# Performance work log

Measured on AMD Instinct MI355X. Metric: run time of the kernel, lower is better.

## Reference

```python
import jax, jax.numpy as jnp
import numpy as np

B, T, E, H, QKV = 4, 2048, 1024, 16, 64
D = E // H  # head_dim = 64


def setup_inputs() -> dict:
    key = jax.random.key(0)
    k1, k2, k3, k4 = jax.random.split(key, 4)
    scale = 1.0 / np.sqrt(D)
    x = jax.random.normal(k1, (B, T, E), dtype=jnp.float32)
    W_q = jax.random.normal(k2, (QKV, D), dtype=jnp.float32) * scale
    W_k = jax.random.normal(k3, (QKV, D), dtype=jnp.float32) * scale
    W_v = jax.random.normal(k4, (QKV, D), dtype=jnp.float32) * scale
    return {"x": x, "W_q": W_q, "W_k": W_k, "W_v": W_v}


def reference(x, W_q, W_k, W_v):
    Bx, Tx, Ex = x.shape
    d = Ex // H
    # [B,T,E] -> [B,H,T,D]  (same as torch view + permute(0,2,1,3))
    xh = x.reshape(Bx, Tx, H, d).transpose(0, 2, 1, 3)
    # Shared per-head projections: Linear(d -> qkv_dim), weight stored [out,in]
    Q = jnp.einsum("bhtd,qd->bhtq", xh, W_q)
    K = jnp.einsum("bhtd,qd->bhtq", xh, W_k)
    V = jnp.einsum("bhtd,qd->bhtq", xh, W_v)
    # NOTE: original scales by head_dim**0.5, not qkv_dim**0.5
    scores = jnp.einsum("bhtq,bhsq->bhts", Q, K) / jnp.asarray(d, x.dtype) ** 0.5
    attn = jax.nn.softmax(scores, axis=-1)
    out = jnp.einsum("bhts,bhsq->bhtq", attn, V) + V  # attention + V residual
    # per-head concat on last dim == head-major merge: [B,H,T,Q] -> [B,T,H*Q]
    return out.transpose(0, 2, 1, 3).reshape(Bx, Tx, H * W_q.shape[0])
```

## Files before the change

### kernel.cpp

```cpp
#include <hip/hip_runtime.h>

#define T_SEQ 2048
#define N_B   4
#define N_H   16
#define D_H   64
#define EMB   1024
#define CSC   0.18033688011f

typedef __attribute__((ext_vector_type(8))) short   vshort8;
typedef __attribute__((ext_vector_type(4))) float   vfloat4;
typedef __attribute__((ext_vector_type(16))) float  vfloat16;

__device__ __forceinline__ ushort f2bf(float f) {
  union { float f; unsigned u; } v; v.f = f;
  unsigned u = v.u;
  return (ushort)((u + 0x7fffu + ((u >> 16) & 1u)) >> 16);
}
__device__ __forceinline__ unsigned pk2bf(float a, float b) {
  return (unsigned)f2bf(a) | ((unsigned)f2bf(b) << 16);
}
__device__ __forceinline__ float bf2f(ushort b) {
  union { unsigned u; float f; } v; v.u = ((unsigned)b) << 16;
  return v.f;
}
__device__ __forceinline__ float fexp2(float x) {
#if __has_builtin(__builtin_amdgcn_exp2f)
  return __builtin_amdgcn_exp2f(x);
#else
  return exp2f(x);
#endif
}
__device__ __forceinline__ unsigned permhi(float hi, float lo) {
  union { float f; unsigned u; } a, b; a.f = hi; b.f = lo;
#if __has_builtin(__builtin_amdgcn_perm)
  return __builtin_amdgcn_perm(a.u, b.u, 0x07060302u);
#else
  return (a.u & 0xFFFF0000u) | (b.u >> 16);
#endif
}
__device__ __forceinline__ vshort8 cvt8(const float* p) {
  float4 w0 = *(const float4*)(p);
  float4 w1 = *(const float4*)(p + 4);
  vshort8 t;
  t[0] = (short)f2bf(w0.x); t[1] = (short)f2bf(w0.y);
  t[2] = (short)f2bf(w0.z); t[3] = (short)f2bf(w0.w);
  t[4] = (short)f2bf(w1.x); t[5] = (short)f2bf(w1.y);
  t[6] = (short)f2bf(w1.z); t[7] = (short)f2bf(w1.w);
  return t;
}


__global__ void wconv(const float* __restrict__ Wq, const float* __restrict__ Wk,
                      const float* __restrict__ Wv, ushort* __restrict__ Wb) {
  const int lane = threadIdx.x & 63;
  const int l15  = lane & 15;
  const int quad = lane >> 4;
  const float* Ws[3] = {Wq, Wk, Wv};
#pragma unroll
  for (int m = 0; m < 3; ++m)
#pragma unroll
    for (int kc = 0; kc < 2; ++kc)
#pragma unroll
      for (int nt = 0; nt < 4; ++nt) {
        vshort8 t = cvt8(Ws[m] + (nt * 16 + l15) * D_H + kc * 32 + quad * 8);
        *(vshort8*)(&Wb[(((m * 2 + kc) * 4 + nt) * 64 + lane) * 8]) = t;
      }
}

__global__ __launch_bounds__(256, 4) void proj_qkv(
    const float* __restrict__ x, const ushort* __restrict__ Wb,
    uint2* __restrict__ Qb, uint2* __restrict__ Kb, uint2* __restrict__ Vb) {
  const int wid  = threadIdx.x >> 6;
  const int lane = threadIdx.x & 63;
  const int l15  = lane & 15;
  const int q    = lane >> 4;
  const int gw    = blockIdx.x * 4 + wid;
  const int strip = gw >> 4;
  const int hd    = gw & 15;
  const int r0    = strip * 16;
  const int b     = r0 >> 11;
  const int bh    = b * N_H + hd;
  const int ts    = (r0 & (T_SEQ - 1)) >> 4;

  vshort8 afr[2];
  {
    const float* xp = x + (size_t)(r0 + l15) * EMB + hd * D_H + q * 8;
    afr[0] = cvt8(xp);
    afr[1] = cvt8(xp + 32);
  }

  uint2* Bs[3] = {Qb, Kb, Vb};
#pragma unroll
  for (int m = 0; m < 3; ++m) {
    vshort8 wf[2][4];
#pragma unroll
    for (int kc = 0; kc < 2; ++kc)
#pragma unroll
      for (int nt = 0; nt < 4; ++nt)
        wf[kc][nt] = *(const vshort8*)(&Wb[(((m * 2 + kc) * 4 + nt) * 64 + lane) * 8]);
    vfloat4 acc[4];
#pragma unroll
    for (int nt = 0; nt < 4; ++nt) acc[nt] = (vfloat4){0.f, 0.f, 0.f, 0.f};
#pragma unroll
    for (int kc = 0; kc < 2; ++kc)
#pragma unroll
      for (int nt = 0; nt < 4; ++nt)
        acc[nt] = (m < 2)
          ? __builtin_amdgcn_mfma_f32_16x16x32_bf16(wf[kc][nt], afr[kc], acc[nt], 0, 0, 0)
          : __builtin_amdgcn_mfma_f32_16x16x32_bf16(afr[kc], wf[kc][nt], acc[nt], 0, 0, 0);
    uint2* B = Bs[m];
#pragma unroll
    for (int nt = 0; nt < 4; ++nt) {
      vfloat4 a = acc[nt];
      if (m == 0) { a[0] *= CSC; a[1] *= CSC; a[2] *= CSC; a[3] *= CSC; }
      uint2 w;
      w.x = pk2bf(a[0], a[1]);
      w.y = pk2bf(a[2], a[3]);
      size_t idx;
      if (m < 2) {
        idx = ((size_t)(bh * 64 + (ts >> 1)) * 4 + nt) * 128
              + (l15 + 16 * (ts & 1)) * 4 + q;
      } else {
        idx = (((size_t)(bh * 32 + (ts >> 2)) * 4 + (ts & 3)) * 2 + (nt >> 1)) * 128
              + 64 * (nt & 1) + l15 * 4 + q;
      }
      B[idx] = w;
    }
  }
}

__global__ __launch_bounds__(256, 2) void attn_fused(
    const uint4* __restrict__ Qb, const uint4* __restrict__ Kb,
    const uint4* __restrict__ Vb, float* __restrict__ out) {
  const int tid  = threadIdx.x;
  const int wid  = tid >> 6;
  const int lane = tid & 63;
  const int l31  = lane & 31;
  const int h    = lane >> 5;

  const int blk  = blockIdx.x;
  const int work = (blk & 7) * 64 + (blk >> 3);
  const int bh   = work >> 3;
  const int tblk8 = work & 7;
  const int b = bh >> 4, hh = bh & 15;
  const int T64 = tblk8 * 4 + wid;

  const int lo = l31 * 2 + h;

  vshort8 qf[2][4];
#pragma unroll
  for (int tb = 0; tb < 2; ++tb)
#pragma unroll
    for (int ds = 0; ds < 4; ++ds)
      qf[tb][ds] = *(const vshort8*)&Qb[((size_t)(bh * 64 + 2 * T64 + tb) * 4 + ds) * 64 + lo];

  vfloat16 oacc[2][2];
#pragma unroll
  for (int tb = 0; tb < 2; ++tb)
#pragma unroll
    for (int db = 0; db < 2; ++db)
#pragma unroll
      for (int i = 0; i < 16; ++i) oacc[tb][db][i] = 0.f;
  float lsum[2] = {0.f, 0.f};

#pragma unroll 1
  for (int ss = 0; ss < 32; ++ss) {
    vshort8 kf[2][4];
#pragma unroll
    for (int sb = 0; sb < 2; ++sb)
#pragma unroll
      for (int ds = 0; ds < 4; ++ds)
        kf[sb][ds] = *(const vshort8*)&Kb[((size_t)(bh * 64 + 2 * ss + sb) * 4 + ds) * 64 + lo];
    vshort8 vf[4][2];
#pragma unroll
    for (int st = 0; st < 4; ++st)
#pragma unroll
      for (int db = 0; db < 2; ++db)
        vf[st][db] = *(const vshort8*)&Vb[(((size_t)(bh * 32 + ss) * 4 + st) * 2 + db) * 64 + lo];

#pragma unroll
    for (int tb = 0; tb < 2; ++tb) {
      vfloat16 sacc[2];
#pragma unroll
      for (int sb = 0; sb < 2; ++sb) {
#pragma unroll
        for (int i = 0; i < 16; ++i) sacc[sb][i] = 0.f;
#pragma unroll
        for (int ds = 0; ds < 4; ++ds)
          sacc[sb] = __builtin_amdgcn_mfma_f32_32x32x16_bf16(kf[sb][ds], qf[tb][ds], sacc[sb], 0, 0, 0);
      }
      float p[2][16];
      float ls = 0.f;
#pragma unroll
      for (int sb = 0; sb < 2; ++sb)
#pragma unroll
        for (int r = 0; r < 16; ++r) {
          p[sb][r] = fexp2(sacc[sb][r]);
          ls += p[sb][r];
        }
      lsum[tb] += ls;

#pragma unroll
      for (int sb = 0; sb < 2; ++sb)
#pragma unroll
        for (int g = 0; g < 2; ++g) {
          const unsigned OL0 = permhi(p[sb][8 * g + 1], p[sb][8 * g + 0]);
          const unsigned OL1 = permhi(p[sb][8 * g + 3], p[sb][8 * g + 2]);
          const unsigned OH0 = permhi(p[sb][8 * g + 5], p[sb][8 * g + 4]);
          const unsigned OH1 = permhi(p[sb][8 * g + 7], p[sb][8 * g + 6]);
          const unsigned s0 = h ? OL0 : OH0;
          const unsigned s1 = h ? OL1 : OH1;
          const unsigned r0 = (unsigned)__shfl_xor((int)s0, 32, 64);
          const unsigned r1 = (unsigned)__shfl_xor((int)s1, 32, 64);
          union { unsigned u[4]; vshort8 v; } pa;
          pa.u[0] = h ? r0 : OL0;
          pa.u[1] = h ? r1 : OL1;
          pa.u[2] = h ? OH0 : r0;
          pa.u[3] = h ? OH1 : r1;
          const int st = 2 * sb + g;
#pragma unroll
          for (int db = 0; db < 2; ++db)
            oacc[tb][db] = __builtin_amdgcn_mfma_f32_32x32x16_bf16(pa.v, vf[st][db], oacc[tb][db], 0, 0, 0);
        }
    }
  }

  const uint2* Vb2 = (const uint2*)Vb;
#pragma unroll
  for (int tb = 0; tb < 2; ++tb) {
    const float l = lsum[tb] + __shfl_xor(lsum[tb], 32, 64);
    const float inv = 1.0f / l;
    const int T32 = 2 * T64 + tb;
#pragma unroll
    for (int db = 0; db < 2; ++db) {
#pragma unroll
      for (int rq = 0; rq < 4; ++rq) {
        const int sq = 8 * T32 + 2 * rq + h;
        uint2 vr = Vb2[(((size_t)(bh * 32 + (sq >> 4)) * 4 + ((sq >> 2) & 3)) * 2 + db) * 128
                       + l31 * 4 + ((sq >> 1) & 1) * 2 + (sq & 1)];
        float vres[4];
        vres[0] = bf2f((ushort)(vr.x & 0xFFFFu));
        vres[1] = bf2f((ushort)(vr.x >> 16));
        vres[2] = bf2f((ushort)(vr.y & 0xFFFFu));
        vres[3] = bf2f((ushort)(vr.y >> 16));
#pragma unroll
        for (int rr = 0; rr < 4; ++rr) {
          const int row = rr + 8 * rq + 4 * h;
          const float iT = __shfl(inv, row, 64);
          const int t = T32 * 32 + row;
          out[((size_t)(b * T_SEQ + t)) * EMB + hh * D_H + db * 32 + l31] =
              oacc[tb][db][rq * 4 + rr] * iT + vres[rr];
        }
      }
    }
  }
}

extern "C" void kernel_launch(void* const* d_in, const int* in_sizes, int n_in,
                              void* d_out, int out_size, void* d_ws, size_t ws_size,
                              hipStream_t stream) {
  const float* x  = (const float*)d_in[0];
  const float* Wq = (const float*)d_in[1];
  const float* Wk = (const float*)d_in[2];
  const float* Wv = (const float*)d_in[3];
  float* out = (float*)d_out;

  const size_t per4 = (size_t)64 * 64 * 4 * 64;
  uint4* Qb = (uint4*)d_ws;
  uint4* Kb = Qb + per4;
  uint4* Vb = Kb + per4;
  ushort* Wb = (ushort*)(Vb + per4);

  wconv<<<1, 64, 0, stream>>>(Wq, Wk, Wv, Wb);
  proj_qkv<<<2048, 256, 0, stream>>>(x, Wb, (uint2*)Qb, (uint2*)Kb, (uint2*)Vb);
  attn_fused<<<512, 256, 0, stream>>>(Qb, Kb, Vb, out);
}
```

Baseline: 175.8 us.

## Halve per-wave query tile, double grid, use permlane32 swap and setprio

Each wave now processes one 32-row query tile instead of two, and the grid doubles to 1024 blocks with launch bounds raised to 3 blocks per CU. The goals are lower register pressure, higher occupancy and finer load balance. The cross-half shuffle of probabilities is replaced by v_permlane32_swap, and s_setprio wraps the MFMA groups to favour matrix issue. The cost is that each K/V tile loaded per wave is now reused for half as many query rows, which doubles K/V global traffic.

```diff
diff --git a/kernel.cpp b/kernel.cpp
--- a/kernel.cpp
+++ b/kernel.cpp
@@ -37,6 +37,9 @@
 #else
   return (a.u & 0xFFFF0000u) | (b.u >> 16);
 #endif
+}
+__device__ __forceinline__ void plswap(unsigned &a, unsigned &b) {
+  asm("v_permlane32_swap_b32 %0, %1" : "+v"(a), "+v"(b));
 }
 __device__ __forceinline__ vshort8 cvt8(const float* p) {
   float4 w0 = *(const float4*)(p);
@@ -129,7 +132,7 @@
   }
 }
 
-__global__ __launch_bounds__(256, 2) void attn_fused(
+__global__ __launch_bounds__(256, 3) void attn_fused(
     const uint4* __restrict__ Qb, const uint4* __restrict__ Kb,
     const uint4* __restrict__ Vb, float* __restrict__ out) {
   const int tid  = threadIdx.x;
@@ -139,29 +142,25 @@
   const int h    = lane >> 5;
 
   const int blk  = blockIdx.x;
-  const int work = (blk & 7) * 64 + (blk >> 3);
-  const int bh   = work >> 3;
-  const int tblk8 = work & 7;
+  const int work = (blk & 7) * 128 + (blk >> 3);
+  const int bh   = work >> 4;
+  const int tblk = work & 15;
   const int b = bh >> 4, hh = bh & 15;
-  const int T64 = tblk8 * 4 + wid;
+  const int T32 = tblk * 4 + wid;
 
   const int lo = l31 * 2 + h;
 
-  vshort8 qf[2][4];
-#pragma unroll
-  for (int tb = 0; tb < 2; ++tb)
-#pragma unroll
-    for (int ds = 0; ds < 4; ++ds)
-      qf[tb][ds] = *(const vshort8*)&Qb[((size_t)(bh * 64 + 2 * T64 + tb) * 4 + ds) * 64 + lo];
-
-  vfloat16 oacc[2][2];
-#pragma unroll
-  for (int tb = 0; tb < 2; ++tb)
-#pragma unroll
-    for (int db = 0; db < 2; ++db)
-#pragma unroll
-      for (int i = 0; i < 16; ++i) oacc[tb][db][i] = 0.f;
-  float lsum[2] = {0.f, 0.f};
+  vshort8 qf[4];
+#pragma unroll
+  for (int ds = 0; ds < 4; ++ds)
+    qf[ds] = *(const vshort8*)&Qb[((size_t)(bh * 64 + T32) * 4 + ds) * 64 + lo];
+
+  vfloat16 oacc[2];
+#pragma unroll
+  for (int db = 0; db < 2; ++db)
+#pragma unroll
+    for (int i = 0; i < 16; ++i) oacc[db][i] = 0.f;
+  float lsum = 0.f;
 
 #pragma unroll 1
   for (int ss = 0; ss < 32; ++ss) {
@@ -179,78 +178,69 @@
         vf[st][db] = *(const vshort8*)&Vb[(((size_t)(bh * 32 + ss) * 4 + st) * 2 + db) * 64 + lo];
 
 #pragma unroll
-    for (int tb = 0; tb < 2; ++tb) {
-      vfloat16 sacc[2];
-#pragma unroll
-      for (int sb = 0; sb < 2; ++sb) {
-#pragma unroll
-        for (int i = 0; i < 16; ++i) sacc[sb][i] = 0.f;
-#pragma unroll
-        for (int ds = 0; ds < 4; ++ds)
-          sacc[sb] = __builtin_amdgcn_mfma_f32_32x32x16_bf16(kf[sb][ds], qf[tb][ds], sacc[sb], 0, 0, 0);
-      }
-      float p[2][16];
-      float ls = 0.f;
-#pragma unroll
-      for (int sb = 0; sb < 2; ++sb)
-#pragma unroll
-        for (int r = 0; r < 16; ++r) {
-          p[sb][r] = fexp2(sacc[sb][r]);
-          ls += p[sb][r];
-        }
-      lsum[tb] += ls;
-
-#pragma unroll
-      for (int sb = 0; sb < 2; ++sb)
-#pragma unroll
-        for (int g = 0; g < 2; ++g) {
-          const unsigned OL0 = permhi(p[sb][8 * g + 1], p[sb][8 * g + 0]);
-          const unsigned OL1 = permhi(p[sb][8 * g + 3], p[sb][8 * g + 2]);
-          const unsigned OH0 = permhi(p[sb][8 * g + 5], p[sb][8 * g + 4]);
-          const unsigned OH1 = permhi(p[sb][8 * g + 7], p[sb][8 * g + 6]);
-          const unsigned s0 = h ? OL0 : OH0;
-          const unsigned s1 = h ? OL1 : OH1;
-          const unsigned r0 = (unsigned)__shfl_xor((int)s0, 32, 64);
-          const unsigned r1 = (unsigned)__shfl_xor((int)s1, 32, 64);
-          union { unsigned u[4]; vshort8 v; } pa;
-          pa.u[0] = h ? r0 : OL0;
-          pa.u[1] = h ? r1 : OL1;
-          pa.u[2] = h ? OH0 : r0;
-          pa.u[3] = h ? OH1 : r1;
-          const int st = 2 * sb + g;
-#pragma unroll
-          for (int db = 0; db < 2; ++db)
-            oacc[tb][db] = __builtin_amdgcn_mfma_f32_32x32x16_bf16(pa.v, vf[st][db], oacc[tb][db], 0, 0, 0);
-        }
+    for (int sb = 0; sb < 2; ++sb) {
+      vfloat16 sacc;
+#pragma unroll
+      for (int i = 0; i < 16; ++i) sacc[i] = 0.f;
+      __builtin_amdgcn_s_setprio(1);
+#pragma unroll
+      for (int ds = 0; ds < 4; ++ds)
+        sacc = __builtin_amdgcn_mfma_f32_32x32x16_bf16(kf[sb][ds], qf[ds], sacc, 0, 0, 0);
+      __builtin_amdgcn_s_setprio(0);
+
+      float p[16];
+      float s0 = 0.f, s1 = 0.f, s2 = 0.f, s3 = 0.f;
+#pragma unroll
+      for (int r = 0; r < 16; r += 4) {
+        p[r + 0] = fexp2(sacc[r + 0]); s0 += p[r + 0];
+        p[r + 1] = fexp2(sacc[r + 1]); s1 += p[r + 1];
+        p[r + 2] = fexp2(sacc[r + 2]); s2 += p[r + 2];
+        p[r + 3] = fexp2(sacc[r + 3]); s3 += p[r + 3];
+      }
+      lsum += (s0 + s1) + (s2 + s3);
+
+#pragma unroll
+      for (int g = 0; g < 2; ++g) {
+        unsigned OL0 = permhi(p[8 * g + 1], p[8 * g + 0]);
+        unsigned OL1 = permhi(p[8 * g + 3], p[8 * g + 2]);
+        unsigned OH0 = permhi(p[8 * g + 5], p[8 * g + 4]);
+        unsigned OH1 = permhi(p[8 * g + 7], p[8 * g + 6]);
+        plswap(OL0, OH0);
+        plswap(OL1, OH1);
+        union { unsigned u[4]; vshort8 v; } pa;
+        pa.u[0] = OL0; pa.u[1] = OL1; pa.u[2] = OH0; pa.u[3] = OH1;
+        const int st = 2 * sb + g;
+        __builtin_amdgcn_s_setprio(1);
+#pragma unroll
+        for (int db = 0; db < 2; ++db)
+          oacc[db] = __builtin_amdgcn_mfma_f32_32x32x16_bf16(pa.v, vf[st][db], oacc[db], 0, 0, 0);
+        __builtin_amdgcn_s_setprio(0);
+      }
     }
   }
 
   const uint2* Vb2 = (const uint2*)Vb;
-#pragma unroll
-  for (int tb = 0; tb < 2; ++tb) {
-    const float l = lsum[tb] + __shfl_xor(lsum[tb], 32, 64);
-    const float inv = 1.0f / l;
-    const int T32 = 2 * T64 + tb;
-#pragma unroll
-    for (int db = 0; db < 2; ++db) {
-#pragma unroll
-      for (int rq = 0; rq < 4; ++rq) {
-        const int sq = 8 * T32 + 2 * rq + h;
-        uint2 vr = Vb2[(((size_t)(bh * 32 + (sq >> 4)) * 4 + ((sq >> 2) & 3)) * 2 + db) * 128
-                       + l31 * 4 + ((sq >> 1) & 1) * 2 + (sq & 1)];
-        float vres[4];
-        vres[0] = bf2f((ushort)(vr.x & 0xFFFFu));
-        vres[1] = bf2f((ushort)(vr.x >> 16));
-        vres[2] = bf2f((ushort)(vr.y & 0xFFFFu));
-        vres[3] = bf2f((ushort)(vr.y >> 16));
-#pragma unroll
-        for (int rr = 0; rr < 4; ++rr) {
-          const int row = rr + 8 * rq + 4 * h;
-          const float iT = __shfl(inv, row, 64);
-          const int t = T32 * 32 + row;
-          out[((size_t)(b * T_SEQ + t)) * EMB + hh * D_H + db * 32 + l31] =
-              oacc[tb][db][rq * 4 + rr] * iT + vres[rr];
-        }
+  const float l = lsum + __shfl_xor(lsum, 32, 64);
+  const float inv = 1.0f / l;
+#pragma unroll
+  for (int db = 0; db < 2; ++db) {
+#pragma unroll
+    for (int rq = 0; rq < 4; ++rq) {
+      const int sq = 8 * T32 + 2 * rq + h;
+      uint2 vr = Vb2[(((size_t)(bh * 32 + (sq >> 4)) * 4 + ((sq >> 2) & 3)) * 2 + db) * 128
+                     + l31 * 4 + ((sq >> 1) & 1) * 2 + (sq & 1)];
+      float vres[4];
+      vres[0] = bf2f((ushort)(vr.x & 0xFFFFu));
+      vres[1] = bf2f((ushort)(vr.x >> 16));
+      vres[2] = bf2f((ushort)(vr.y & 0xFFFFu));
+      vres[3] = bf2f((ushort)(vr.y >> 16));
+#pragma unroll
+      for (int rr = 0; rr < 4; ++rr) {
+        const int row = rr + 8 * rq + 4 * h;
+        const float iT = __shfl(inv, row, 64);
+        const int t = T32 * 32 + row;
+        out[((size_t)(b * T_SEQ + t)) * EMB + hh * D_H + db * 32 + l31] =
+            oacc[db][rq * 4 + rr] * iT + vres[rr];
       }
     }
   }
@@ -273,5 +263,5 @@
 
   wconv<<<1, 64, 0, stream>>>(Wq, Wk, Wv, Wb);
   proj_qkv<<<2048, 256, 0, stream>>>(x, Wb, (uint2*)Qb, (uint2*)Kb, (uint2*)Vb);
-  attn_fused<<<512, 256, 0, stream>>>(Qb, Kb, Vb, out);
-}
+  attn_fused<<<1024, 256, 0, stream>>>(Qb, Kb, Vb, out);
+}
```

Result: slower. 182.8 us (+4.0%).

## Split key range across wave pairs, reduce partials via LDS, use permlane swap

Applied to the files above, without the earlier changes.

Each block now covers two 64-row query chunks instead of four. Each chunk's key loop is split between two waves, and the halves are combined through shared memory before the epilogue, which doubles the grid to 1024 blocks and raises launch bounds to 3 blocks per SM. The cross-half shuffle and selects are replaced by v_permlane32_swap, s_setprio is placed around the MFMA groups, and the row-sum accumulation is split into four independent chains. The aim is more parallelism and occupancy on the attention kernel, at the cost of an LDS reduction, a barrier and tighter register limits.

```diff
diff --git a/kernel.cpp b/kernel.cpp
--- a/kernel.cpp
+++ b/kernel.cpp
@@ -37,6 +37,9 @@
 #else
   return (a.u & 0xFFFF0000u) | (b.u >> 16);
 #endif
+}
+__device__ __forceinline__ void plswap(unsigned &a, unsigned &b) {
+  asm("v_permlane32_swap_b32 %0, %1" : "+v"(a), "+v"(b));
 }
 __device__ __forceinline__ vshort8 cvt8(const float* p) {
   float4 w0 = *(const float4*)(p);
@@ -129,7 +132,7 @@
   }
 }
 
-__global__ __launch_bounds__(256, 2) void attn_fused(
+__global__ __launch_bounds__(256, 3) void attn_fused(
     const uint4* __restrict__ Qb, const uint4* __restrict__ Kb,
     const uint4* __restrict__ Vb, float* __restrict__ out) {
   const int tid  = threadIdx.x;
@@ -137,13 +140,15 @@
   const int lane = tid & 63;
   const int l31  = lane & 31;
   const int h    = lane >> 5;
+  const int chunk = wid & 1;
+  const int sh    = wid >> 1;
 
   const int blk  = blockIdx.x;
-  const int work = (blk & 7) * 64 + (blk >> 3);
-  const int bh   = work >> 3;
-  const int tblk8 = work & 7;
+  const int work = (blk & 7) * 128 + (blk >> 3);
+  const int bh   = work >> 4;
+  const int tblk = work & 15;
   const int b = bh >> 4, hh = bh & 15;
-  const int T64 = tblk8 * 4 + wid;
+  const int T64 = tblk * 2 + chunk;
 
   const int lo = l31 * 2 + h;
 
@@ -164,7 +169,7 @@
   float lsum[2] = {0.f, 0.f};
 
 #pragma unroll 1
-  for (int ss = 0; ss < 32; ++ss) {
+  for (int ss = sh * 16; ss < sh * 16 + 16; ++ss) {
     vshort8 kf[2][4];
 #pragma unroll
     for (int sb = 0; sb < 2; ++sb)
@@ -182,74 +187,104 @@
     for (int tb = 0; tb < 2; ++tb) {
       vfloat16 sacc[2];
 #pragma unroll
-      for (int sb = 0; sb < 2; ++sb) {
+      for (int sb = 0; sb < 2; ++sb)
 #pragma unroll
         for (int i = 0; i < 16; ++i) sacc[sb][i] = 0.f;
+      __builtin_amdgcn_s_setprio(1);
+#pragma unroll
+      for (int sb = 0; sb < 2; ++sb)
 #pragma unroll
         for (int ds = 0; ds < 4; ++ds)
           sacc[sb] = __builtin_amdgcn_mfma_f32_32x32x16_bf16(kf[sb][ds], qf[tb][ds], sacc[sb], 0, 0, 0);
-      }
+      __builtin_amdgcn_s_setprio(0);
+
       float p[2][16];
-      float ls = 0.f;
+      float s0 = 0.f, s1 = 0.f, s2 = 0.f, s3 = 0.f;
 #pragma unroll
       for (int sb = 0; sb < 2; ++sb)
 #pragma unroll
-        for (int r = 0; r < 16; ++r) {
-          p[sb][r] = fexp2(sacc[sb][r]);
-          ls += p[sb][r];
+        for (int r = 0; r < 16; r += 4) {
+          p[sb][r + 0] = fexp2(sacc[sb][r + 0]); s0 += p[sb][r + 0];
+          p[sb][r + 1] = fexp2(sacc[sb][r + 1]); s1 += p[sb][r + 1];
+          p[sb][r + 2] = fexp2(sacc[sb][r + 2]); s2 += p[sb][r + 2];
+          p[sb][r + 3] = fexp2(sacc[sb][r + 3]); s3 += p[sb][r + 3];
         }
-      lsum[tb] += ls;
+      lsum[tb] += (s0 + s1) + (s2 + s3);
 
 #pragma unroll
       for (int sb = 0; sb < 2; ++sb)
 #pragma unroll
         for (int g = 0; g < 2; ++g) {
-          const unsigned OL0 = permhi(p[sb][8 * g + 1], p[sb][8 * g + 0]);
-          const unsigned OL1 = permhi(p[sb][8 * g + 3], p[sb][8 * g + 2]);
-          const unsigned OH0 = permhi(p[sb][8 * g + 5], p[sb][8 * g + 4]);
-          const unsigned OH1 = permhi(p[sb][8 * g + 7], p[sb][8 * g + 6]);
-          const unsigned s0 = h ? OL0 : OH0;
-          const unsigned s1 = h ? OL1 : OH1;
-          const unsigned r0 = (unsigned)__shfl_xor((int)s0, 32, 64);
-          const unsigned r1 = (unsigned)__shfl_xor((int)s1, 32, 64);
+          unsigned OL0 = permhi(p[sb][8 * g + 1], p[sb][8 * g + 0]);
+          unsigned OL1 = permhi(p[sb][8 * g + 3], p[sb][8 * g + 2]);
+          unsigned OH0 = permhi(p[sb][8 * g + 5], p[sb][8 * g + 4]);
+          unsigned OH1 = permhi(p[sb][8 * g + 7], p[sb][8 * g + 6]);
+          plswap(OL0, OH0);
+          plswap(OL1, OH1);
           union { unsigned u[4]; vshort8 v; } pa;
-          pa.u[0] = h ? r0 : OL0;
-          pa.u[1] = h ? r1 : OL1;
-          pa.u[2] = h ? OH0 : r0;
-          pa.u[3] = h ? OH1 : r1;
+          pa.u[0] = OL0; pa.u[1] = OL1; pa.u[2] = OH0; pa.u[3] = OH1;
           const int st = 2 * sb + g;
+          __builtin_amdgcn_s_setprio(1);
 #pragma unroll
           for (int db = 0; db < 2; ++db)
             oacc[tb][db] = __builtin_amdgcn_mfma_f32_32x32x16_bf16(pa.v, vf[st][db], oacc[tb][db], 0, 0, 0);
+          __builtin_amdgcn_s_setprio(0);
         }
     }
   }
 
-  const uint2* Vb2 = (const uint2*)Vb;
-#pragma unroll
-  for (int tb = 0; tb < 2; ++tb) {
-    const float l = lsum[tb] + __shfl_xor(lsum[tb], 32, 64);
-    const float inv = 1.0f / l;
-    const int T32 = 2 * T64 + tb;
-#pragma unroll
-    for (int db = 0; db < 2; ++db) {
-#pragma unroll
-      for (int rq = 0; rq < 4; ++rq) {
-        const int sq = 8 * T32 + 2 * rq + h;
-        uint2 vr = Vb2[(((size_t)(bh * 32 + (sq >> 4)) * 4 + ((sq >> 2) & 3)) * 2 + db) * 128
-                       + l31 * 4 + ((sq >> 1) & 1) * 2 + (sq & 1)];
-        float vres[4];
-        vres[0] = bf2f((ushort)(vr.x & 0xFFFFu));
-        vres[1] = bf2f((ushort)(vr.x >> 16));
-        vres[2] = bf2f((ushort)(vr.y & 0xFFFFu));
-        vres[3] = bf2f((ushort)(vr.y >> 16));
-#pragma unroll
-        for (int rr = 0; rr < 4; ++rr) {
-          const int row = rr + 8 * rq + 4 * h;
-          const float iT = __shfl(inv, row, 64);
-          const int t = T32 * 32 + row;
-          out[((size_t)(b * T_SEQ + t)) * EMB + hh * D_H + db * 32 + l31] =
-              oacc[tb][db][rq * 4 + rr] * iT + vres[rr];
+  __shared__ float sO[2][64][64];
+  __shared__ float sL[2][2][64];
+  if (sh == 0) {
+#pragma unroll
+    for (int tb = 0; tb < 2; ++tb) {
+      sL[chunk][tb][lane] = lsum[tb];
+#pragma unroll
+      for (int db = 0; db < 2; ++db)
+#pragma unroll
+        for (int i = 0; i < 16; ++i)
+          sO[chunk][(tb * 2 + db) * 16 + i][lane] = oacc[tb][db][i];
+    }
+  }
+  __syncthreads();
+
+  if (sh == 1) {
+#pragma unroll
+    for (int tb = 0; tb < 2; ++tb) {
+      lsum[tb] += sL[chunk][tb][lane];
+#pragma unroll
+      for (int db = 0; db < 2; ++db)
+#pragma unroll
+        for (int i = 0; i < 16; ++i)
+          oacc[tb][db][i] += sO[chunk][(tb * 2 + db) * 16 + i][lane];
+    }
+
+    const uint2* Vb2 = (const uint2*)Vb;
+#pragma unroll
+    for (int tb = 0; tb < 2; ++tb) {
+      const float l = lsum[tb] + __shfl_xor(lsum[tb], 32, 64);
+      const float inv = 1.0f / l;
+      const int T32 = 2 * T64 + tb;
+#pragma unroll
+      for (int db = 0; db < 2; ++db) {
+#pragma unroll
+        for (int rq = 0; rq < 4; ++rq) {
+          const int sq = 8 * T32 + 2 * rq + h;
+          uint2 vr = Vb2[(((size_t)(bh * 32 + (sq >> 4)) * 4 + ((sq >> 2) & 3)) * 2 + db) * 128
+                         + l31 * 4 + ((sq >> 1) & 1) * 2 + (sq & 1)];
+          float vres[4];
+          vres[0] = bf2f((ushort)(vr.x & 0xFFFFu));
+          vres[1] = bf2f((ushort)(vr.x >> 16));
+          vres[2] = bf2f((ushort)(vr.y & 0xFFFFu));
+          vres[3] = bf2f((ushort)(vr.y >> 16));
+#pragma unroll
+          for (int rr = 0; rr < 4; ++rr) {
+            const int row = rr + 8 * rq + 4 * h;
+            const float iT = __shfl(inv, row, 64);
+            const int t = T32 * 32 + row;
+            out[((size_t)(b * T_SEQ + t)) * EMB + hh * D_H + db * 32 + l31] =
+                oacc[tb][db][rq * 4 + rr] * iT + vres[rr];
+          }
         }
       }
     }
@@ -273,5 +308,5 @@
 
   wconv<<<1, 64, 0, stream>>>(Wq, Wk, Wv, Wb);
   proj_qkv<<<2048, 256, 0, stream>>>(x, Wb, (uint2*)Qb, (uint2*)Kb, (uint2*)Vb);
-  attn_fused<<<512, 256, 0, stream>>>(Qb, Kb, Vb, out);
-}
+  attn_fused<<<1024, 256, 0, stream>>>(Qb, Kb, Vb, out);
+}
```

Measured after the change: 645.4 us. 3.67x slower.

## Use permlane32 swap for P repack, add setprio around MFMAs, unroll KV loop

Applied to the files above, without the earlier changes.

Replaces the ds_swizzle/shuffle-based cross-half exchange of the bf16 probability fragments with a v_permlane32_swap instruction, dropping the selects and LDS-path shuffles. It also wraps the MFMA groups in s_setprio to favor matrix issue across waves, and unrolls the KV loop by two with incremented pointers. The first MFMA now takes a zero accumulator instead of explicit zeroing, and the row-sum uses four partial accumulators. It relies on gfx950 permlane32_swap semantics matching the old selection logic and raises register pressure from the unroll.

```diff
diff --git a/kernel.cpp b/kernel.cpp
--- a/kernel.cpp
+++ b/kernel.cpp
@@ -37,6 +37,9 @@
 #else
   return (a.u & 0xFFFF0000u) | (b.u >> 16);
 #endif
+}
+__device__ __forceinline__ void plswap(unsigned &a, unsigned &b) {
+  asm("v_permlane32_swap_b32 %0, %1" : "+v"(a), "+v"(b));
 }
 __device__ __forceinline__ vshort8 cvt8(const float* p) {
   float4 w0 = *(const float4*)(p);
@@ -163,64 +166,77 @@
       for (int i = 0; i < 16; ++i) oacc[tb][db][i] = 0.f;
   float lsum[2] = {0.f, 0.f};
 
-#pragma unroll 1
+  vfloat16 vzero;
+#pragma unroll
+  for (int i = 0; i < 16; ++i) vzero[i] = 0.f;
+
+  const uint4* kp0 = Kb + ((size_t)(bh * 64) * 4) * 64 + lo;
+  const uint4* kp1 = kp0 + 256;
+  const uint4* vp0 = Vb + ((size_t)(bh * 32) * 8) * 64 + lo;
+  const uint4* vp1 = vp0 + 256;
+
+#pragma unroll 2
   for (int ss = 0; ss < 32; ++ss) {
     vshort8 kf[2][4];
 #pragma unroll
-    for (int sb = 0; sb < 2; ++sb)
-#pragma unroll
-      for (int ds = 0; ds < 4; ++ds)
-        kf[sb][ds] = *(const vshort8*)&Kb[((size_t)(bh * 64 + 2 * ss + sb) * 4 + ds) * 64 + lo];
+    for (int ds = 0; ds < 4; ++ds) {
+      kf[0][ds] = *(const vshort8*)&kp0[ds * 64];
+      kf[1][ds] = *(const vshort8*)&kp1[ds * 64];
+    }
     vshort8 vf[4][2];
 #pragma unroll
-    for (int st = 0; st < 4; ++st)
-#pragma unroll
-      for (int db = 0; db < 2; ++db)
-        vf[st][db] = *(const vshort8*)&Vb[(((size_t)(bh * 32 + ss) * 4 + st) * 2 + db) * 64 + lo];
+    for (int st = 0; st < 2; ++st)
+#pragma unroll
+      for (int db = 0; db < 2; ++db) {
+        vf[st][db]     = *(const vshort8*)&vp0[(st * 2 + db) * 64];
+        vf[st + 2][db] = *(const vshort8*)&vp1[(st * 2 + db) * 64];
+      }
+    kp0 += 512; kp1 += 512; vp0 += 512; vp1 += 512;
 
 #pragma unroll
     for (int tb = 0; tb < 2; ++tb) {
       vfloat16 sacc[2];
+      __builtin_amdgcn_s_setprio(1);
 #pragma unroll
       for (int sb = 0; sb < 2; ++sb) {
-#pragma unroll
-        for (int i = 0; i < 16; ++i) sacc[sb][i] = 0.f;
-#pragma unroll
-        for (int ds = 0; ds < 4; ++ds)
+        sacc[sb] = __builtin_amdgcn_mfma_f32_32x32x16_bf16(kf[sb][0], qf[tb][0], vzero, 0, 0, 0);
+#pragma unroll
+        for (int ds = 1; ds < 4; ++ds)
           sacc[sb] = __builtin_amdgcn_mfma_f32_32x32x16_bf16(kf[sb][ds], qf[tb][ds], sacc[sb], 0, 0, 0);
       }
+      __builtin_amdgcn_s_setprio(0);
+
       float p[2][16];
-      float ls = 0.f;
+      float s0 = 0.f, s1 = 0.f, s2 = 0.f, s3 = 0.f;
 #pragma unroll
       for (int sb = 0; sb < 2; ++sb)
 #pragma unroll
-        for (int r = 0; r < 16; ++r) {
-          p[sb][r] = fexp2(sacc[sb][r]);
-          ls += p[sb][r];
+        for (int r = 0; r < 16; r += 4) {
+          p[sb][r + 0] = fexp2(sacc[sb][r + 0]); s0 += p[sb][r + 0];
+          p[sb][r + 1] = fexp2(sacc[sb][r + 1]); s1 += p[sb][r + 1];
+          p[sb][r + 2] = fexp2(sacc[sb][r + 2]); s2 += p[sb][r + 2];
+          p[sb][r + 3] = fexp2(sacc[sb][r + 3]); s3 += p[sb][r + 3];
         }
-      lsum[tb] += ls;
+      lsum[tb] += (s0 + s1) + (s2 + s3);
 
 #pragma unroll
       for (int sb = 0; sb < 2; ++sb)
 #pragma unroll
         for (int g = 0; g < 2; ++g) {
-          const unsigned OL0 = permhi(p[sb][8 * g + 1], p[sb][8 * g + 0]);
-          const unsigned OL1 = permhi(p[sb][8 * g + 3], p[sb][8 * g + 2]);
-          const unsigned OH0 = permhi(p[sb][8 * g + 5], p[sb][8 * g + 4]);
-          const unsigned OH1 = permhi(p[sb][8 * g + 7], p[sb][8 * g + 6]);
-          const unsigned s0 = h ? OL0 : OH0;
-          const unsigned s1 = h ? OL1 : OH1;
-          const unsigned r0 = (unsigned)__shfl_xor((int)s0, 32, 64);
-          const unsigned r1 = (unsigned)__shfl_xor((int)s1, 32, 64);
+          unsigned OL0 = permhi(p[sb][8 * g + 1], p[sb][8 * g + 0]);
+          unsigned OL1 = permhi(p[sb][8 * g + 3], p[sb][8 * g + 2]);
+          unsigned OH0 = permhi(p[sb][8 * g + 5], p[sb][8 * g + 4]);
+          unsigned OH1 = permhi(p[sb][8 * g + 7], p[sb][8 * g + 6]);
+          plswap(OL0, OH0);
+          plswap(OL1, OH1);
           union { unsigned u[4]; vshort8 v; } pa;
-          pa.u[0] = h ? r0 : OL0;
-          pa.u[1] = h ? r1 : OL1;
-          pa.u[2] = h ? OH0 : r0;
-          pa.u[3] = h ? OH1 : r1;
+          pa.u[0] = OL0; pa.u[1] = OL1; pa.u[2] = OH0; pa.u[3] = OH1;
           const int st = 2 * sb + g;
+          __builtin_amdgcn_s_setprio(1);
 #pragma unroll
           for (int db = 0; db < 2; ++db)
             oacc[tb][db] = __builtin_amdgcn_mfma_f32_32x32x16_bf16(pa.v, vf[st][db], oacc[tb][db], 0, 0, 0);
+          __builtin_amdgcn_s_setprio(0);
         }
     }
   }
```

New measurement: 190.8 us. +8.5%, slower.
